# Performance work log

Measured on AMD Instinct MI355X. Metric: run time of the kernel, lower is better.

The kernel has to match this reference:

```python
import jax, jax.numpy as jnp
import numpy as np

IN_DIM = 1024
HID = 1024
DEPTH = 13            # perfect binary tree: 2**13 = 8192 leaves, 8191 internal nodes
N_LEAVES = 2 ** DEPTH
N_TOKENS = 8192
N_OPS = 4             # '+', '/', '*', '-' (ordered_op=False)


def setup_inputs() -> dict:
    key = jax.random.key(0)
    ks = jax.random.split(key, 16)
    sW = 1.0 / np.sqrt(IN_DIM)
    sU = 1.0 / np.sqrt(HID)
    inp = {
        "tokens": jax.random.normal(ks[0], (N_TOKENS, IN_DIM), jnp.float32),
        "leaf_token_ids": jax.random.randint(ks[1], (N_LEAVES,), 0, N_TOKENS),
        "op_ids": jax.random.randint(ks[2], (N_LEAVES - 1,), 0, N_OPS),
        "W_i": jax.random.normal(ks[3], (HID, IN_DIM), jnp.float32) * sW,
        "W_o": jax.random.normal(ks[4], (HID, IN_DIM), jnp.float32) * sW,
        "W_u": jax.random.normal(ks[5], (HID, IN_DIM), jnp.float32) * sW,
        "W_f": jax.random.normal(ks[6], (HID, IN_DIM), jnp.float32) * sW,
        "U_i": jax.random.normal(ks[7], (HID, HID), jnp.float32) * sU,
        "U_o": jax.random.normal(ks[8], (HID, HID), jnp.float32) * sU,
        "U_u": jax.random.normal(ks[9], (HID, HID), jnp.float32) * sU,
        "U_f": jax.random.normal(ks[10], (HID, HID), jnp.float32) * sU,
        "b_i": jnp.zeros((1, HID), jnp.float32),
        "b_o": jnp.zeros((1, HID), jnp.float32),
        "b_u": jnp.zeros((1, HID), jnp.float32),
        "b_f": jnp.zeros((1, HID), jnp.float32),
        "op_emb": jax.random.uniform(ks[11], (N_OPS, IN_DIM), jnp.float32, -1.0, 1.0),
        "c_init": jnp.zeros((2, HID), jnp.float32),
        "h_init": jnp.zeros((2, HID), jnp.float32),
    }
    return inp


def reference(tokens, leaf_token_ids, op_ids, W_i, W_o, W_u, W_f,
              U_i, U_o, U_u, U_f, b_i, b_o, b_u, b_f,
              op_emb, c_init, h_init):
    """Depth-batched Child-Sum TreeLSTM over a perfect binary tree.
    op_ids are stored root-first level order: level l (root=0) occupies
    op_ids[2**l - 1 : 2**(l+1) - 1]. Leaves are level DEPTH.
    Children of node j at level l are nodes 2j, 2j+1 at level l+1.
    Returns jnp.stack([c_root, h_root])  -> [2, 1, HID]."""
    H = U_i.shape[0]

    def node_step(x, c_state, h_state):
        # x: [n, in_dim]; c_state/h_state: [n, 2, H]
        h_sum = h_state.sum(axis=1)                                   # [n, H]
        i = jax.nn.sigmoid(x @ W_i.T + h_sum @ U_i.T + b_i)
        o = jax.nn.sigmoid(x @ W_o.T + h_sum @ U_o.T + b_o)
        u = jnp.tanh(x @ W_u.T + h_sum @ U_u.T + b_u)
        f = jax.nn.sigmoid((x @ W_f.T)[:, None, :] + h_state @ U_f.T + b_f)  # [n,2,H]
        c = i * u + (f * c_state).sum(axis=1)                         # [n, H]
        h = o * jnp.tanh(c)
        return c, h

    n = leaf_token_ids.shape[0]
    depth = int(np.log2(n))
    # leaves: learnable init states, x = embedding of the token
    x = tokens[leaf_token_ids]                                        # [n, in_dim]
    c, h = node_step(x,
                     jnp.broadcast_to(c_init, (n, 2, H)),
                     jnp.broadcast_to(h_init, (n, 2, H)))
    # internal levels, bottom-up
    for l in range(depth - 1, -1, -1):
        m = 2 ** l
        off = m - 1
        x = op_emb[op_ids[off:off + m]]                               # [m, in_dim]
        c, h = node_step(x, c.reshape(m, 2, H), h.reshape(m, 2, H))
    return jnp.stack([c, h])  # [2, 1, H]: root (c, h)
```

## Files before the change

kernel.cpp:

```cpp
#include <hip/hip_runtime.h>

typedef unsigned short u16;
typedef __attribute__((ext_vector_type(4))) unsigned short us4;
typedef __attribute__((ext_vector_type(4))) float f4;
typedef __attribute__((ext_vector_type(8))) short bf16x8;
typedef __attribute__((ext_vector_type(4))) float f32x4;

__device__ __forceinline__ u16 f2bf(float x) {
  unsigned u = __float_as_uint(x);
  return (u16)((u + 0x7FFFu + ((u >> 16) & 1u)) >> 16);
}
__device__ __forceinline__ float b2f(u16 s) {
  return __uint_as_float(((unsigned)s) << 16);
}
__device__ __forceinline__ float sigm(float x) { return 1.f / (1.f + __expf(-x)); }
__device__ __forceinline__ float tanhf_(float x) { return 2.f / (1.f + __expf(-2.f * x)) - 1.f; }

__global__ void convert_wu_kernel(const float* __restrict__ w0, const float* __restrict__ w1,
                                  const float* __restrict__ w2, const float* __restrict__ w3,
                                  const float* __restrict__ u0, const float* __restrict__ u1,
                                  const float* __restrict__ u2, const float* __restrict__ u3,
                                  u16* __restrict__ Wb, u16* __restrict__ Ub) {
  int mat = blockIdx.x >> 10;
  int off4 = (int)(blockIdx.x & 1023) * 256 + threadIdx.x;
  const float* src; u16* dst;
  switch (mat) {
    case 0: src = w0; dst = Wb; break;
    case 1: src = w1; dst = Wb + 1048576; break;
    case 2: src = w2; dst = Wb + 2097152; break;
    case 3: src = w3; dst = Wb + 3145728; break;
    case 4: src = u0; dst = Ub; break;
    case 5: src = u1; dst = Ub + 1048576; break;
    case 6: src = u2; dst = Ub + 2097152; break;
    default: src = u3; dst = Ub + 3145728; break;
  }
  f4 v = ((const f4*)src)[off4];
  us4 o = {f2bf(v[0]), f2bf(v[1]), f2bf(v[2]), f2bf(v[3])};
  ((us4*)dst)[off4] = o;
}

__global__ void gather_leaf_kernel(const float* __restrict__ tokens,
                                   const int* __restrict__ ids, u16* __restrict__ Xl) {
  int n = blockIdx.x, t = threadIdx.x;
  int tok = ids[n];
  f4 v = ((const f4*)(tokens + (size_t)tok * 1024))[t];
  us4 o = {f2bf(v[0]), f2bf(v[1]), f2bf(v[2]), f2bf(v[3])};
  ((us4*)(Xl + (size_t)n * 1024))[t] = o;
}

__global__ void precompute_kernel(const float* __restrict__ op_emb,
    const float* __restrict__ w0, const float* __restrict__ w1,
    const float* __restrict__ w2, const float* __restrict__ w3,
    const float* __restrict__ u0, const float* __restrict__ u1,
    const float* __restrict__ u2, const float* __restrict__ u3,
    const float* __restrict__ b0, const float* __restrict__ b1,
    const float* __restrict__ b2, const float* __restrict__ b3,
    const float* __restrict__ h_init,
    float* __restrict__ xw, float* __restrict__ leafC) {
  int id = blockIdx.x * 256 + threadIdx.x;
  if (id < 16384) {
    int op = id >> 12, g = (id >> 10) & 3, j = id & 1023;
    const float* wsrc; const float* bs;
    switch (g) {
      case 0: wsrc = w0; bs = b0; break;
      case 1: wsrc = w1; bs = b1; break;
      case 2: wsrc = w2; bs = b2; break;
      default: wsrc = w3; bs = b3; break;
    }
    const f4* xr = (const f4*)(op_emb + (size_t)op * 1024);
    const f4* wr = (const f4*)(wsrc + (size_t)j * 1024);
    float s = bs[j];
    for (int k = 0; k < 256; ++k) {
      f4 a = xr[k], b = wr[k];
      s += a[0] * b[0] + a[1] * b[1] + a[2] * b[2] + a[3] * b[3];
    }
    xw[id] = s;
  } else if (id < 21504) {
    int id2 = id - 16384;
    int sel = id2 >> 10, j = id2 & 1023;
    const f4* h0 = (const f4*)h_init;
    const f4* h1 = (const f4*)(h_init + 1024);
    float s;
    if (sel < 3) {
      const float* usrc; const float* bs;
      switch (sel) {
        case 0: usrc = u0; bs = b0; break;
        case 1: usrc = u1; bs = b1; break;
        default: usrc = u2; bs = b2; break;
      }
      const f4* wr = (const f4*)(usrc + (size_t)j * 1024);
      s = bs[j];
      for (int k = 0; k < 256; ++k) {
        f4 a0 = h0[k], a1 = h1[k], b = wr[k];
        s += (a0[0] + a1[0]) * b[0] + (a0[1] + a1[1]) * b[1] +
             (a0[2] + a1[2]) * b[2] + (a0[3] + a1[3]) * b[3];
      }
    } else {
      const f4* hs = (sel == 3) ? h0 : h1;
      const f4* wr = (const f4*)(u3 + (size_t)j * 1024);
      s = b3[j];
      for (int k = 0; k < 256; ++k) {
        f4 a = hs[k], b = wr[k];
        s += a[0] * b[0] + a[1] * b[1] + a[2] * b[2] + a[3] * b[3];
      }
    }
    leafC[id2] = s;
  }
}

template <int NRT, int NCT>
__global__ __launch_bounds__(256, (NRT == 8 ? 2 : 3)) void tree_gemm(
    const u16* __restrict__ A, const u16* __restrict__ Wm,
    const float* __restrict__ consts,
    const int* __restrict__ ops,
    const float* __restrict__ c_in,
    float* __restrict__ c_out, u16* __restrict__ h_out,
    int nrows, int m_parents, int is_leaf, float* __restrict__ out_root) {
  constexpr int ROWS = NRT * 16;
  constexpr int COLS = NCT * 16;
  constexpr int S = 64 / NCT;
  constexpr int LOG2S = (NCT == 2 ? 5 : 4);
  constexpr int NST = NRT / 2;
  constexpr int DBUF = NRT * 2048;
  constexpr int PASSES = (NRT == 8 ? 2 : 1);
  constexpr int RPP = ROWS / PASSES;
  constexpr int FPP = RPP / 16;
  constexpr int SMEM_U16 =
      (4 * RPP * 68 > NRT * 2048 ? 4 * RPP * 68 : NRT * 2048);
  __shared__ __align__(16) u16 smem[SMEM_U16];
  char* smem_c = (char*)smem;

  const int tid = threadIdx.x;
  const int wave = tid >> 6;
  const int lane = tid & 63;
  const int stripe = blockIdx.x & (S - 1);
  const int rowblk = blockIdx.x >> LOG2S;
  const int r0 = rowblk * ROWS;
  const int j0 = stripe * COLS;
  const int ln15 = lane & 15, quad = lane >> 4;
  const int sub = lane >> 3, gsel = lane & 7;

  const char* pAsrc[NST];
  unsigned a_dst[NST];
#pragma unroll
  for (int i = 0; i < NST; ++i) {
    int slot = (wave * NST + i) * 8 + sub;
    int row = r0 + slot; if (row >= nrows) row = nrows - 1;
    pAsrc[i] = (const char*)(A + (size_t)row * 1024 + (unsigned)((gsel ^ sub) * 8));
    a_dst[i] = (unsigned)((wave * NST + i) * 1024 + lane * 16);
  }
  const char* pB[NCT];
#pragma unroll
  for (int f = 0; f < NCT; ++f)
    pB[f] = (const char*)(Wm + (size_t)(wave * 1024 + j0 + f * 16 + ln15) * 1024 + quad * 8);

  unsigned a_base[2];
#pragma unroll
  for (int ks = 0; ks < 2; ++ks)
    a_base[ks] = (unsigned)(ln15 * 128 + (((ks * 4 + quad) ^ (ln15 & 7)) * 16));

  f32x4 acc[NRT][NCT];
#pragma unroll
  for (int t = 0; t < NRT; ++t)
#pragma unroll
    for (int f = 0; f < NCT; ++f) acc[t][f] = (f32x4){0.f, 0.f, 0.f, 0.f};

#pragma unroll
  for (int i = 0; i < NST; ++i)
    __builtin_amdgcn_global_load_lds(
        (const __attribute__((address_space(1))) void*)(pAsrc[i]),
        (__attribute__((address_space(3))) void*)(smem_c + a_dst[i]), 16, 0, 0);
  bf16x8 bcur[2][NCT], bnxt[2][NCT];
#pragma unroll
  for (int ks = 0; ks < 2; ++ks)
#pragma unroll
    for (int f = 0; f < NCT; ++f)
      bcur[ks][f] = *(const bf16x8*)(pB[f] + ks * 64);

#pragma unroll
  for (int ch = 0; ch < 16; ++ch) {
    __syncthreads();
    if (ch < 15) {
#pragma unroll
      for (int i = 0; i < NST; ++i)
        __builtin_amdgcn_global_load_lds(
            (const __attribute__((address_space(1))) void*)(pAsrc[i] + (ch + 1) * 128),
            (__attribute__((address_space(3))) void*)(smem_c + ((ch + 1) & 1) * DBUF + a_dst[i]),
            16, 0, 0);
#pragma unroll
      for (int ks = 0; ks < 2; ++ks)
#pragma unroll
        for (int f = 0; f < NCT; ++f)
          bnxt[ks][f] = *(const bf16x8*)(pB[f] + (ch + 1) * 128 + ks * 64);
    }
    const unsigned cb = (unsigned)((ch & 1) * DBUF);
    {
      bf16x8 af[NRT];
#pragma unroll
      for (int t = 0; t < NRT; ++t)
        af[t] = *(const bf16x8*)(smem_c + cb + a_base[0] + t * 2048);
#pragma unroll
      for (int t = 0; t < NRT; ++t)
#pragma unroll
        for (int f = 0; f < NCT; ++f)
          acc[t][f] = __builtin_amdgcn_mfma_f32_16x16x32_bf16(af[t], bcur[0][f],
                                                              acc[t][f], 0, 0, 0);
    }
    {
      bf16x8 af[NRT];
#pragma unroll
      for (int t = 0; t < NRT; ++t)
        af[t] = *(const bf16x8*)(smem_c + cb + a_base[1] + t * 2048);
#pragma unroll
      for (int t = 0; t < NRT; ++t)
#pragma unroll
        for (int f = 0; f < NCT; ++f)
          acc[t][f] = __builtin_amdgcn_mfma_f32_16x16x32_bf16(af[t], bcur[1][f],
                                                              acc[t][f], 0, 0, 0);
    }
#pragma unroll
    for (int ks = 0; ks < 2; ++ks)
#pragma unroll
      for (int f = 0; f < NCT; ++f) bcur[ks][f] = bnxt[ks][f];
  }

#pragma unroll
  for (int pass = 0; pass < PASSES; ++pass) {
    __syncthreads();
#pragma unroll
    for (int tt = 0; tt < FPP; ++tt) {
      int t = pass * FPP + tt;
#pragma unroll
      for (int f = 0; f < NCT; ++f)
#pragma unroll
        for (int k = 0; k < 4; ++k) {
          int row = tt * 16 + quad * 4 + k;
          int col = f * 16 + ln15;
          smem[(wave * RPP + row) * 68 + col] = f2bf(acc[t][f][k]);
        }
    }
    __syncthreads();
    const int rbase = r0 + pass * RPP;

    if (is_leaf) {
      for (int e = tid; e < RPP * COLS; e += 256) {
        int r = e / COLS, j = e % COLS;
        int col = j0 + j, n = rbase + r;
        float p0 = b2f(smem[(0 * RPP + r) * 68 + j]);
        float p1 = b2f(smem[(1 * RPP + r) * 68 + j]);
        float p2 = b2f(smem[(2 * RPP + r) * 68 + j]);
        float p3 = b2f(smem[(3 * RPP + r) * 68 + j]);
        float i_ = sigm(p0 + consts[col]);
        float o_ = sigm(p1 + consts[1024 + col]);
        float u_ = tanhf_(p2 + consts[2048 + col]);
        float f0 = sigm(p3 + consts[3072 + col]);
        float f1 = sigm(p3 + consts[4096 + col]);
        float c = i_ * u_ + f0 * c_in[col] + f1 * c_in[1024 + col];
        float h = o_ * tanhf_(c);
        c_out[(size_t)n * 1024 + col] = c;
        h_out[(size_t)n * 1024 + col] = f2bf(h);
      }
    } else {
      for (int e = tid; e < (RPP / 2) * COLS; e += 256) {
        int p = e / COLS, j = e % COLS;
        int np = (rbase >> 1) + p;
        if (np >= m_parents) break;
        int col = j0 + j;
        int op = ops[np];
        const float* xwop = consts + ((unsigned)(op * 4) << 10);
        float p0a = b2f(smem[(0 * RPP + 2 * p) * 68 + j]), p0b = b2f(smem[(0 * RPP + 2 * p + 1) * 68 + j]);
        float p1a = b2f(smem[(1 * RPP + 2 * p) * 68 + j]), p1b = b2f(smem[(1 * RPP + 2 * p + 1) * 68 + j]);
        float p2a = b2f(smem[(2 * RPP + 2 * p) * 68 + j]), p2b = b2f(smem[(2 * RPP + 2 * p + 1) * 68 + j]);
        float p3a = b2f(smem[(3 * RPP + 2 * p) * 68 + j]), p3b = b2f(smem[(3 * RPP + 2 * p + 1) * 68 + j]);
        float i_ = sigm(p0a + p0b + xwop[col]);
        float o_ = sigm(p1a + p1b + xwop[1024 + col]);
        float u_ = tanhf_(p2a + p2b + xwop[2048 + col]);
        float f0 = sigm(p3a + xwop[3072 + col]);
        float f1 = sigm(p3b + xwop[3072 + col]);
        float c = i_ * u_ + f0 * c_in[(size_t)(rbase + 2 * p) * 1024 + col]
                          + f1 * c_in[(size_t)(rbase + 2 * p + 1) * 1024 + col];
        float h = o_ * tanhf_(c);
        if (m_parents == 1) {
          out_root[col] = c;
          out_root[1024 + col] = h;
        } else {
          c_out[(size_t)np * 1024 + col] = c;
          h_out[(size_t)np * 1024 + col] = f2bf(h);
        }
      }
    }
  }
}

extern "C" void kernel_launch(void* const* d_in, const int* in_sizes, int n_in,
                              void* d_out, int out_size, void* d_ws, size_t ws_size,
                              hipStream_t stream) {
  const float* tokens = (const float*)d_in[0];
  const int* leaf_ids = (const int*)d_in[1];
  const int* op_ids = (const int*)d_in[2];
  const float* W0 = (const float*)d_in[3];
  const float* W1 = (const float*)d_in[4];
  const float* W2 = (const float*)d_in[5];
  const float* W3 = (const float*)d_in[6];
  const float* U0 = (const float*)d_in[7];
  const float* U1 = (const float*)d_in[8];
  const float* U2 = (const float*)d_in[9];
  const float* U3 = (const float*)d_in[10];
  const float* B0 = (const float*)d_in[11];
  const float* B1 = (const float*)d_in[12];
  const float* B2 = (const float*)d_in[13];
  const float* B3 = (const float*)d_in[14];
  const float* op_emb = (const float*)d_in[15];
  const float* c_init = (const float*)d_in[16];
  const float* h_init = (const float*)d_in[17];
  float* out = (float*)d_out;

  char* ws = (char*)d_ws;
  u16* Wb = (u16*)ws;
  u16* Ub = Wb + (size_t)4 * 1024 * 1024;
  u16* Xl = Ub + (size_t)4 * 1024 * 1024;
  u16* hA = Xl + (size_t)8192 * 1024;
  u16* hB = hA + (size_t)8192 * 1024;
  float* cA = (float*)(hB + (size_t)4096 * 1024);
  float* cB = cA + (size_t)8192 * 1024;
  float* xw = cB + (size_t)4096 * 1024;
  float* lc = xw + 16 * 1024;

  convert_wu_kernel<<<8192, 256, 0, stream>>>(W0, W1, W2, W3, U0, U1, U2, U3, Wb, Ub);
  gather_leaf_kernel<<<8192, 256, 0, stream>>>(tokens, leaf_ids, Xl);
  precompute_kernel<<<84, 256, 0, stream>>>(op_emb, W0, W1, W2, W3, U0, U1, U2, U3,
                                            B0, B1, B2, B3, h_init, xw, lc);

  tree_gemm<8, 2><<<64 * 32, 256, 0, stream>>>(Xl, Wb, lc, nullptr, c_init,
                                               cA, hA, 8192, 0, 1, out);

  const u16* hin = hA; const float* cin = cA;
  u16* hout = hB; float* cout = cB;
  for (int l = 12; l >= 0; --l) {
    int m = 1 << l;
    int nrows = 2 * m;
    if (nrows >= 2048) {
      tree_gemm<8, 2><<<(nrows / 128) * 32, 256, 0, stream>>>(
          hin, Ub, xw, op_ids + (m - 1), cin, cout, hout, nrows, m, 0, out);
    } else if (nrows >= 1024) {
      tree_gemm<4, 2><<<(nrows / 64) * 32, 256, 0, stream>>>(
          hin, Ub, xw, op_ids + (m - 1), cin, cout, hout, nrows, m, 0, out);
    } else {
      int rg = nrows / 32; if (rg < 1) rg = 1;
      tree_gemm<2, 2><<<rg * 32, 256, 0, stream>>>(
          hin, Ub, xw, op_ids + (m - 1), cin, cout, hout, nrows, m, 0, out);
    }
    const u16* th = hin; hin = hout; hout = (u16*)th;
    const float* tc = cin; cin = cout; cout = (float*)tc;
  }
}
```

Measured before the change: 602.6 us.

## Merge setup kernels, split epilogue into more passes, move B prefetch after first MFMA

Combines the weight conversion, leaf gather and precompute kernels into one launch with block-range dispatch, removing two kernel launches and their serialization gaps. Increases epilogue passes for the 8- and 4-row-tile GEMM variants, which shrinks the shared-memory staging area and may improve occupancy at the cost of more passes. Moves the next-chunk B-fragment global loads to after the first MFMA half so they overlap compute and reduce register pressure.

```diff
diff --git a/kernel.cpp b/kernel.cpp
--- a/kernel.cpp
+++ b/kernel.cpp
@@ -16,95 +16,91 @@
 __device__ __forceinline__ float sigm(float x) { return 1.f / (1.f + __expf(-x)); }
 __device__ __forceinline__ float tanhf_(float x) { return 2.f / (1.f + __expf(-2.f * x)) - 1.f; }
 
-__global__ void convert_wu_kernel(const float* __restrict__ w0, const float* __restrict__ w1,
-                                  const float* __restrict__ w2, const float* __restrict__ w3,
-                                  const float* __restrict__ u0, const float* __restrict__ u1,
-                                  const float* __restrict__ u2, const float* __restrict__ u3,
-                                  u16* __restrict__ Wb, u16* __restrict__ Ub) {
-  int mat = blockIdx.x >> 10;
-  int off4 = (int)(blockIdx.x & 1023) * 256 + threadIdx.x;
-  const float* src; u16* dst;
-  switch (mat) {
-    case 0: src = w0; dst = Wb; break;
-    case 1: src = w1; dst = Wb + 1048576; break;
-    case 2: src = w2; dst = Wb + 2097152; break;
-    case 3: src = w3; dst = Wb + 3145728; break;
-    case 4: src = u0; dst = Ub; break;
-    case 5: src = u1; dst = Ub + 1048576; break;
-    case 6: src = u2; dst = Ub + 2097152; break;
-    default: src = u3; dst = Ub + 3145728; break;
-  }
-  f4 v = ((const f4*)src)[off4];
-  us4 o = {f2bf(v[0]), f2bf(v[1]), f2bf(v[2]), f2bf(v[3])};
-  ((us4*)dst)[off4] = o;
-}
-
-__global__ void gather_leaf_kernel(const float* __restrict__ tokens,
-                                   const int* __restrict__ ids, u16* __restrict__ Xl) {
-  int n = blockIdx.x, t = threadIdx.x;
-  int tok = ids[n];
-  f4 v = ((const f4*)(tokens + (size_t)tok * 1024))[t];
-  us4 o = {f2bf(v[0]), f2bf(v[1]), f2bf(v[2]), f2bf(v[3])};
-  ((us4*)(Xl + (size_t)n * 1024))[t] = o;
-}
-
-__global__ void precompute_kernel(const float* __restrict__ op_emb,
+__global__ void setup_kernel(
+    const float* __restrict__ tokens, const int* __restrict__ leaf_ids,
     const float* __restrict__ w0, const float* __restrict__ w1,
     const float* __restrict__ w2, const float* __restrict__ w3,
     const float* __restrict__ u0, const float* __restrict__ u1,
     const float* __restrict__ u2, const float* __restrict__ u3,
     const float* __restrict__ b0, const float* __restrict__ b1,
     const float* __restrict__ b2, const float* __restrict__ b3,
-    const float* __restrict__ h_init,
+    const float* __restrict__ op_emb, const float* __restrict__ h_init,
+    u16* __restrict__ Wb, u16* __restrict__ Ub, u16* __restrict__ Xl,
     float* __restrict__ xw, float* __restrict__ leafC) {
-  int id = blockIdx.x * 256 + threadIdx.x;
-  if (id < 16384) {
-    int op = id >> 12, g = (id >> 10) & 3, j = id & 1023;
-    const float* wsrc; const float* bs;
-    switch (g) {
-      case 0: wsrc = w0; bs = b0; break;
-      case 1: wsrc = w1; bs = b1; break;
-      case 2: wsrc = w2; bs = b2; break;
-      default: wsrc = w3; bs = b3; break;
-    }
-    const f4* xr = (const f4*)(op_emb + (size_t)op * 1024);
-    const f4* wr = (const f4*)(wsrc + (size_t)j * 1024);
-    float s = bs[j];
-    for (int k = 0; k < 256; ++k) {
-      f4 a = xr[k], b = wr[k];
-      s += a[0] * b[0] + a[1] * b[1] + a[2] * b[2] + a[3] * b[3];
-    }
-    xw[id] = s;
-  } else if (id < 21504) {
-    int id2 = id - 16384;
-    int sel = id2 >> 10, j = id2 & 1023;
-    const f4* h0 = (const f4*)h_init;
-    const f4* h1 = (const f4*)(h_init + 1024);
-    float s;
-    if (sel < 3) {
-      const float* usrc; const float* bs;
-      switch (sel) {
-        case 0: usrc = u0; bs = b0; break;
-        case 1: usrc = u1; bs = b1; break;
-        default: usrc = u2; bs = b2; break;
-      }
-      const f4* wr = (const f4*)(usrc + (size_t)j * 1024);
-      s = bs[j];
+  const int bid = blockIdx.x;
+  if (bid < 8192) {
+    int mat = bid >> 10;
+    int off4 = (int)(bid & 1023) * 256 + threadIdx.x;
+    const float* src; u16* dst;
+    switch (mat) {
+      case 0: src = w0; dst = Wb; break;
+      case 1: src = w1; dst = Wb + 1048576; break;
+      case 2: src = w2; dst = Wb + 2097152; break;
+      case 3: src = w3; dst = Wb + 3145728; break;
+      case 4: src = u0; dst = Ub; break;
+      case 5: src = u1; dst = Ub + 1048576; break;
+      case 6: src = u2; dst = Ub + 2097152; break;
+      default: src = u3; dst = Ub + 3145728; break;
+    }
+    f4 v = ((const f4*)src)[off4];
+    us4 o = {f2bf(v[0]), f2bf(v[1]), f2bf(v[2]), f2bf(v[3])};
+    ((us4*)dst)[off4] = o;
+  } else if (bid < 16384) {
+    int n = bid - 8192, t = threadIdx.x;
+    int tok = leaf_ids[n];
+    f4 v = ((const f4*)(tokens + (size_t)tok * 1024))[t];
+    us4 o = {f2bf(v[0]), f2bf(v[1]), f2bf(v[2]), f2bf(v[3])};
+    ((us4*)(Xl + (size_t)n * 1024))[t] = o;
+  } else {
+    int id = (bid - 16384) * 256 + threadIdx.x;
+    if (id < 16384) {
+      int op = id >> 12, g = (id >> 10) & 3, j = id & 1023;
+      const float* wsrc; const float* bs;
+      switch (g) {
+        case 0: wsrc = w0; bs = b0; break;
+        case 1: wsrc = w1; bs = b1; break;
+        case 2: wsrc = w2; bs = b2; break;
+        default: wsrc = w3; bs = b3; break;
+      }
+      const f4* xr = (const f4*)(op_emb + (size_t)op * 1024);
+      const f4* wr = (const f4*)(wsrc + (size_t)j * 1024);
+      float s = bs[j];
       for (int k = 0; k < 256; ++k) {
-        f4 a0 = h0[k], a1 = h1[k], b = wr[k];
-        s += (a0[0] + a1[0]) * b[0] + (a0[1] + a1[1]) * b[1] +
-             (a0[2] + a1[2]) * b[2] + (a0[3] + a1[3]) * b[3];
-      }
-    } else {
-      const f4* hs = (sel == 3) ? h0 : h1;
-      const f4* wr = (const f4*)(u3 + (size_t)j * 1024);
-      s = b3[j];
-      for (int k = 0; k < 256; ++k) {
-        f4 a = hs[k], b = wr[k];
+        f4 a = xr[k], b = wr[k];
         s += a[0] * b[0] + a[1] * b[1] + a[2] * b[2] + a[3] * b[3];
       }
-    }
-    leafC[id2] = s;
+      xw[id] = s;
+    } else if (id < 21504) {
+      int id2 = id - 16384;
+      int sel = id2 >> 10, j = id2 & 1023;
+      const f4* h0 = (const f4*)h_init;
+      const f4* h1 = (const f4*)(h_init + 1024);
+      float s;
+      if (sel < 3) {
+        const float* usrc; const float* bs;
+        switch (sel) {
+          case 0: usrc = u0; bs = b0; break;
+          case 1: usrc = u1; bs = b1; break;
+          default: usrc = u2; bs = b2; break;
+        }
+        const f4* wr = (const f4*)(usrc + (size_t)j * 1024);
+        s = bs[j];
+        for (int k = 0; k < 256; ++k) {
+          f4 a0 = h0[k], a1 = h1[k], b = wr[k];
+          s += (a0[0] + a1[0]) * b[0] + (a0[1] + a1[1]) * b[1] +
+               (a0[2] + a1[2]) * b[2] + (a0[3] + a1[3]) * b[3];
+        }
+      } else {
+        const f4* hs = (sel == 3) ? h0 : h1;
+        const f4* wr = (const f4*)(u3 + (size_t)j * 1024);
+        s = b3[j];
+        for (int k = 0; k < 256; ++k) {
+          f4 a = hs[k], b = wr[k];
+          s += a[0] * b[0] + a[1] * b[1] + a[2] * b[2] + a[3] * b[3];
+        }
+      }
+      leafC[id2] = s;
+    }
   }
 }
 
@@ -122,7 +118,7 @@
   constexpr int LOG2S = (NCT == 2 ? 5 : 4);
   constexpr int NST = NRT / 2;
   constexpr int DBUF = NRT * 2048;
-  constexpr int PASSES = (NRT == 8 ? 2 : 1);
+  constexpr int PASSES = (NRT == 8 ? 4 : (NRT == 4 ? 2 : 1));
   constexpr int RPP = ROWS / PASSES;
   constexpr int FPP = RPP / 16;
   constexpr int SMEM_U16 =
@@ -187,11 +183,6 @@
             (const __attribute__((address_space(1))) void*)(pAsrc[i] + (ch + 1) * 128),
             (__attribute__((address_space(3))) void*)(smem_c + ((ch + 1) & 1) * DBUF + a_dst[i]),
             16, 0, 0);
-#pragma unroll
-      for (int ks = 0; ks < 2; ++ks)
-#pragma unroll
-        for (int f = 0; f < NCT; ++f)
-          bnxt[ks][f] = *(const bf16x8*)(pB[f] + (ch + 1) * 128 + ks * 64);
     }
     const unsigned cb = (unsigned)((ch & 1) * DBUF);
     {
@@ -205,6 +196,13 @@
         for (int f = 0; f < NCT; ++f)
           acc[t][f] = __builtin_amdgcn_mfma_f32_16x16x32_bf16(af[t], bcur[0][f],
                                                               acc[t][f], 0, 0, 0);
+    }
+    if (ch < 15) {
+#pragma unroll
+      for (int ks = 0; ks < 2; ++ks)
+#pragma unroll
+        for (int f = 0; f < NCT; ++f)
+          bnxt[ks][f] = *(const bf16x8*)(pB[f] + (ch + 1) * 128 + ks * 64);
     }
     {
       bf16x8 af[NRT];
@@ -326,10 +324,10 @@
   float* xw = cB + (size_t)4096 * 1024;
   float* lc = xw + 16 * 1024;
 
-  convert_wu_kernel<<<8192, 256, 0, stream>>>(W0, W1, W2, W3, U0, U1, U2, U3, Wb, Ub);
-  gather_leaf_kernel<<<8192, 256, 0, stream>>>(tokens, leaf_ids, Xl);
-  precompute_kernel<<<84, 256, 0, stream>>>(op_emb, W0, W1, W2, W3, U0, U1, U2, U3,
-                                            B0, B1, B2, B3, h_init, xw, lc);
+  setup_kernel<<<16468, 256, 0, stream>>>(tokens, leaf_ids,
+                                          W0, W1, W2, W3, U0, U1, U2, U3,
+                                          B0, B1, B2, B3, op_emb, h_init,
+                                          Wb, Ub, Xl, xw, lc);
 
   tree_gemm<8, 2><<<64 * 32, 256, 0, stream>>>(Xl, Wb, lc, nullptr, c_init,
                                                cA, hA, 8192, 0, 1, out);
```

Result: slower. 670.2 us (+11.2%).
